# Optimization experiments

Measured on AMD Instinct MI355X. Metric: run time of the kernel, lower is better.

Reference implementation:

```python
import jax, jax.numpy as jnp
import numpy as np

B, D, L, E, H = 8192, 1024, 256, 16, 400

def setup_inputs() -> dict:
    key = jax.random.key(0)
    ks = jax.random.split(key, 6)
    s1 = 1.0 / np.sqrt(D)
    s2 = 1.0 / np.sqrt(H)
    return {
        "x": jax.random.normal(ks[0], (B, D), dtype=jnp.float32),
        "angle_idx": jax.random.randint(ks[1], (B,), 0, E, dtype=jnp.int64),
        "W1": jax.random.uniform(ks[2], (E, D, H), jnp.float32, -s1, s1),
        "b1": jax.random.uniform(ks[3], (E, H), jnp.float32, -s1, s1),
        "W2": jax.random.uniform(ks[4], (E, H, 2 * L), jnp.float32, -s2, s2),
        "b2": jax.random.uniform(ks[5], (E, 2 * L), jnp.float32, -s2, s2),
    }

def reference(x, angle_idx, W1, b1, W2, b2):
    # Dense all-experts compute, then per-sample select (jit-friendly MoE dispatch).
    # h1: [E, B, H]
    h1 = jax.nn.relu(jnp.einsum('bd,edh->ebh', x, W1) + b1[:, None, :])
    # h: [E, B, 2L]
    h = jnp.einsum('ebh,ehk->ebk', h1, W2) + b2[:, None, :]
    sel = h[angle_idx, jnp.arange(x.shape[0])]  # [B, 2L], each row from its routed expert
    half = sel.shape[1] // 2
    z_mu, z_logvar = sel[:, :half], sel[:, half:]
    return (z_mu, z_logvar)
```

## Files before the change

### kernel.cpp

```cpp
#include <hip/hip_runtime.h>
#include <hip/hip_bf16.h>
#include <cstdint>
#include <cstddef>

#define B_N 8192
#define D_K 1024
#define H_N 400
#define HP  416
#define K2_N 512
#define E_N 16
#define L_N 256
#define TM 64
#define PAD_ROWS (B_N + E_N * TM)
#define NTILES (PAD_ROWS / TM)

typedef short bf16x8 __attribute__((ext_vector_type(8)));
typedef float f32x4 __attribute__((ext_vector_type(4)));

#define GLDS(gp, lp) __builtin_amdgcn_global_load_lds( \
    (const __attribute__((address_space(1))) unsigned int*)(gp), \
    (__attribute__((address_space(3))) unsigned int*)(lp), 16, 0, 0)

static __device__ __forceinline__ unsigned short f2bf(float f) {
  union { float f; unsigned int u; } c; c.f = f;
  unsigned int u = c.u + 0x7fffu + ((c.u >> 16) & 1u);
  return (unsigned short)(u >> 16);
}
static __device__ __forceinline__ unsigned int pkbf(float a, float b) {
  union { __hip_bfloat162 v; unsigned int u; } c;
  c.v = __float22bfloat162_rn(make_float2(a, b));
  return c.u;
}

__global__ __launch_bounds__(256) void hist_kernel(const int* __restrict__ idx,
                                                   int* __restrict__ hist) {
  __shared__ int h[E_N];
  const int t = threadIdx.x;
  if (t < E_N) h[t] = 0;
  __syncthreads();
  atomicAdd(&h[idx[blockIdx.x * 256 + t]], 1);
  __syncthreads();
  if (t < E_N) hist[blockIdx.x * E_N + t] = h[t];
}

__global__ __launch_bounds__(256) void prep_kernel(const float* __restrict__ W1,
                                                   const float* __restrict__ W2,
                                                   const float* __restrict__ x,
                                                   const int* __restrict__ idx,
                                                   const int* __restrict__ hist,
                                                   unsigned short* __restrict__ Wt1,
                                                   unsigned short* __restrict__ Wt2,
                                                   unsigned short* __restrict__ xc,
                                                   int* __restrict__ off_al,
                                                   int* __restrict__ cnt_al,
                                                   int* __restrict__ order) {
  const int bid = blockIdx.x;
  const int t = threadIdx.x;
  if (bid < 2688) {
    __shared__ unsigned short Ls[64][72];
    const float* S; unsigned short* Dt; int K, N, Kd, Nd, k0, n0;
    if (bid < 1792) {
      int e = bid / 112, r = bid % 112;
      k0 = (r % 16) * 64; n0 = (r / 16) * 64;
      S = W1 + (size_t)e * D_K * H_N; Dt = Wt1 + (size_t)e * HP * D_K;
      K = D_K; N = H_N; Kd = D_K; Nd = HP;
    } else {
      int t2 = bid - 1792; int e = t2 / 56, r = t2 % 56;
      k0 = (r % 7) * 64; n0 = (r / 7) * 64;
      S = W2 + (size_t)e * H_N * K2_N; Dt = Wt2 + (size_t)e * K2_N * HP;
      K = H_N; N = K2_N; Kd = HP; Nd = K2_N;
    }
    const int kk = t >> 4;
    const int nn = (t & 15) * 4;
    float4 v[4];
#pragma unroll
    for (int p = 0; p < 4; ++p) {
      int k = k0 + p * 16 + kk;
      int n = n0 + nn;
      v[p] = make_float4(0.f, 0.f, 0.f, 0.f);
      if (k < K && n + 3 < N) v[p] = *(const float4*)(S + (size_t)k * N + n);
    }
#pragma unroll
    for (int p = 0; p < 4; ++p) {
      Ls[nn + 0][p * 16 + kk] = f2bf(v[p].x);
      Ls[nn + 1][p * 16 + kk] = f2bf(v[p].y);
      Ls[nn + 2][p * 16 + kk] = f2bf(v[p].z);
      Ls[nn + 3][p * 16 + kk] = f2bf(v[p].w);
    }
    __syncthreads();
    const int n2 = t >> 3;
    const int ch = t & 7;
#pragma unroll
    for (int p = 0; p < 2; ++p) {
      int n = n0 + p * 32 + n2;
      int k = k0 + ch * 8;
      if (n < Nd && k < Kd)
        *(uint4*)(Dt + (size_t)n * Kd + k) = *(const uint4*)&Ls[p * 32 + n2][ch * 8];
    }
  } else if (bid < 3200) {
    const int xb = bid - 2688;
    const float* S = x + (size_t)xb * 16 * D_K;
    unsigned short* Dp = xc + (size_t)xb * 16 * D_K;
#pragma unroll
    for (int i = 0; i < 16; ++i) {
      float4 v = *(const float4*)(S + i * D_K + t * 4);
      uint2 o; o.x = pkbf(v.x, v.y); o.y = pkbf(v.z, v.w);
      *(uint2*)(Dp + i * D_K + t * 4) = o;
    }
  } else {
    const int hb = bid - 3200;
    __shared__ int totL[E_N], preL[E_N], offsL[E_N], curL[E_N];
    if (t < E_N) {
      int pre = 0, tot = 0;
      for (int b = 0; b < 32; ++b) {
        int h = hist[b * E_N + t];
        if (b < hb) pre += h;
        tot += h;
      }
      totL[t] = tot; preL[t] = pre;
    }
    __syncthreads();
    if (t == 0) {
      int acc = 0;
      for (int e = 0; e < E_N; ++e) {
        offsL[e] = acc;
        if (hb == 0) off_al[e] = acc;
        acc += ((totL[e] + TM - 1) / TM) * TM;
      }
      if (hb == 0) off_al[E_N] = acc;
    }
    __syncthreads();
    if (t < E_N) {
      curL[t] = offsL[t] + preL[t];
      if (hb == 0) cnt_al[t] = totL[t];
    }
    __syncthreads();
    const int b = hb * 256 + t;
    const int e = idx[b];
    const int slot = atomicAdd(&curL[e], 1);
    order[slot] = b;
    if (hb == 0) *(uint2*)(xc + (size_t)B_N * D_K + t * 4) = make_uint2(0, 0);
  }
}

__global__ __launch_bounds__(256) void gemm1_kernel(const unsigned short* __restrict__ xc,
                                                    const unsigned short* __restrict__ Wt1,
                                                    const float* __restrict__ b1,
                                                    const int* __restrict__ off_al,
                                                    const int* __restrict__ cnt_al,
                                                    const int* __restrict__ order,
                                                    unsigned short* __restrict__ h1buf) {
  __shared__ unsigned short As[2][64 * 32];
  __shared__ unsigned short Bs[2][128 * 32];
  __shared__ int offs[E_N + 1];
  __shared__ int rowidx[TM];
  const int tid = threadIdx.x;
  const int m0 = blockIdx.x * TM;
  const int nb = blockIdx.y;
  if (tid <= E_N) offs[tid] = off_al[tid];
  __syncthreads();
  if (m0 >= offs[E_N]) return;
  int e = 0;
  while (m0 >= offs[e + 1]) ++e;
  if (tid < TM) {
    const bool valid = (m0 + tid) < (offs[e] + cnt_al[e]);
    rowidx[tid] = valid ? order[m0 + tid] : B_N;
  }
  __syncthreads();
  const unsigned short* Wt1e = Wt1 + (size_t)e * HP * D_K;

  const int l = tid & 63, w = tid >> 6;
  const int r4 = l >> 2;
  const int sg = (r4 ^ (r4 >> 2)) & 3;
  const int g8 = ((l & 3) ^ sg) * 8;
  const int t0 = nb * 8 + 2 * w;
  const bool act0 = (t0 < 25);
  const bool act1 = (t0 + 1 < 25);
  const unsigned short* gA = xc + (size_t)rowidx[16 * w + r4] * D_K + g8;
  const unsigned short* gB0 = Wt1e + (size_t)(t0 * 16 + r4) * D_K + g8;
  const unsigned short* gB1 = gB0 + (size_t)16 * D_K;

  const int ln = l & 15, q = l >> 4;
  const int sr = (ln ^ (ln >> 2)) & 3;
  const int cq = (q ^ sr) * 8;

  f32x4 acc[4][2] = {};

  GLDS(gA, &As[0][16 * w * 32]);
  if (act0) GLDS(gB0, &Bs[0][(2 * w + 0) * 512]);
  if (act1) GLDS(gB1, &Bs[0][(2 * w + 1) * 512]);

  for (int k0 = 0; k0 < D_K; k0 += 32) {
    const int cur = (k0 >> 5) & 1;
    const int nxt = cur ^ 1;
    __syncthreads();
    if (k0 + 32 < D_K) {
      GLDS(gA + k0 + 32, &As[nxt][16 * w * 32]);
      if (act0) GLDS(gB0 + k0 + 32, &Bs[nxt][(2 * w + 0) * 512]);
      if (act1) GLDS(gB1 + k0 + 32, &Bs[nxt][(2 * w + 1) * 512]);
    }
    if (act0) {
      bf16x8 af[4];
#pragma unroll
      for (int i = 0; i < 4; ++i)
        af[i] = *(const bf16x8*)&As[cur][(16 * i + ln) * 32 + cq];
      bf16x8 b0f = *(const bf16x8*)&Bs[cur][(2 * w + 0) * 512 + ln * 32 + cq];
#pragma unroll
      for (int i = 0; i < 4; ++i)
        acc[i][0] = __builtin_amdgcn_mfma_f32_16x16x32_bf16(b0f, af[i], acc[i][0], 0, 0, 0);
      if (act1) {
        bf16x8 b1f = *(const bf16x8*)&Bs[cur][(2 * w + 1) * 512 + ln * 32 + cq];
#pragma unroll
        for (int i = 0; i < 4; ++i)
          acc[i][1] = __builtin_amdgcn_mfma_f32_16x16x32_bf16(b1f, af[i], acc[i][1], 0, 0, 0);
      }
    }
  }

#pragma unroll
  for (int j = 0; j < 2; ++j) {
    if (j == 0 ? act0 : act1) {
      const int n4 = (t0 + j) * 16 + 4 * q;
      const float4 bv = *(const float4*)&b1[e * H_N + n4];
#pragma unroll
      for (int i = 0; i < 4; ++i) {
        const size_t m = (size_t)(m0 + 16 * i + ln);
        uint2 o;
        o.x = pkbf(fmaxf(acc[i][j][0] + bv.x, 0.f), fmaxf(acc[i][j][1] + bv.y, 0.f));
        o.y = pkbf(fmaxf(acc[i][j][2] + bv.z, 0.f), fmaxf(acc[i][j][3] + bv.w, 0.f));
        *(uint2*)&h1buf[m * HP + n4] = o;
      }
    }
  }
}

__global__ __launch_bounds__(256) void gemm2_kernel(const unsigned short* __restrict__ h1buf,
                                                    const unsigned short* __restrict__ Wt2,
                                                    const float* __restrict__ b2,
                                                    const int* __restrict__ off_al,
                                                    const int* __restrict__ cnt_al,
                                                    const int* __restrict__ order,
                                                    float* __restrict__ out) {
  __shared__ unsigned short As[2][64 * 32];
  __shared__ unsigned short Bs[2][128 * 32];
  __shared__ int offs[E_N + 1];
  __shared__ int rowidx[TM];
  const int tid = threadIdx.x;
  const int m0 = blockIdx.x * TM;
  const int nb = blockIdx.y;
  if (tid <= E_N) offs[tid] = off_al[tid];
  __syncthreads();
  if (m0 >= offs[E_N]) return;
  int e = 0;
  while (m0 >= offs[e + 1]) ++e;
  if (tid < TM) {
    const bool valid = (m0 + tid) < (offs[e] + cnt_al[e]);
    rowidx[tid] = valid ? order[m0 + tid] : -1;
  }
  __syncthreads();
  const unsigned short* Wt2e = Wt2 + (size_t)e * K2_N * HP;

  const int l = tid & 63, w = tid >> 6;
  const int r4 = l >> 2;
  const int sg = (r4 ^ (r4 >> 2)) & 3;
  const int g8 = ((l & 3) ^ sg) * 8;
  const int t0 = nb * 8 + 2 * w;
  const unsigned short* gA = h1buf + (size_t)(m0 + 16 * w + r4) * HP + g8;
  const unsigned short* gB0 = Wt2e + (size_t)(t0 * 16 + r4) * HP + g8;
  const unsigned short* gB1 = gB0 + (size_t)16 * HP;

  const int ln = l & 15, q = l >> 4;
  const int sr = (ln ^ (ln >> 2)) & 3;
  const int cq = (q ^ sr) * 8;

  f32x4 acc[4][2] = {};

  GLDS(gA, &As[0][16 * w * 32]);
  GLDS(gB0, &Bs[0][(2 * w + 0) * 512]);
  GLDS(gB1, &Bs[0][(2 * w + 1) * 512]);

  for (int k0 = 0; k0 < HP; k0 += 32) {
    const int cur = (k0 >> 5) & 1;
    const int nxt = cur ^ 1;
    __syncthreads();
    if (k0 + 32 < HP) {
      GLDS(gA + k0 + 32, &As[nxt][16 * w * 32]);
      GLDS(gB0 + k0 + 32, &Bs[nxt][(2 * w + 0) * 512]);
      GLDS(gB1 + k0 + 32, &Bs[nxt][(2 * w + 1) * 512]);
    }
    bf16x8 af[4];
#pragma unroll
    for (int i = 0; i < 4; ++i)
      af[i] = *(const bf16x8*)&As[cur][(16 * i + ln) * 32 + cq];
    bf16x8 b0f = *(const bf16x8*)&Bs[cur][(2 * w + 0) * 512 + ln * 32 + cq];
#pragma unroll
    for (int i = 0; i < 4; ++i)
      acc[i][0] = __builtin_amdgcn_mfma_f32_16x16x32_bf16(b0f, af[i], acc[i][0], 0, 0, 0);
    bf16x8 b1f = *(const bf16x8*)&Bs[cur][(2 * w + 1) * 512 + ln * 32 + cq];
#pragma unroll
    for (int i = 0; i < 4; ++i)
      acc[i][1] = __builtin_amdgcn_mfma_f32_16x16x32_bf16(b1f, af[i], acc[i][1], 0, 0, 0);
  }

#pragma unroll
  for (int j = 0; j < 2; ++j) {
    const int n4 = (t0 + j) * 16 + 4 * q;
    const float4 bv = *(const float4*)&b2[e * K2_N + n4];
#pragma unroll
    for (int i = 0; i < 4; ++i) {
      const int s = rowidx[16 * i + ln];
      if (s >= 0) {
        float4 v;
        v.x = acc[i][j][0] + bv.x;
        v.y = acc[i][j][1] + bv.y;
        v.z = acc[i][j][2] + bv.z;
        v.w = acc[i][j][3] + bv.w;
        if (n4 < L_N) *(float4*)&out[(size_t)s * L_N + n4] = v;
        else          *(float4*)&out[(size_t)(B_N + s) * L_N + (n4 - L_N)] = v;
      }
    }
  }
}

extern "C" void kernel_launch(void* const* d_in, const int* in_sizes, int n_in,
                              void* d_out, int out_size, void* d_ws, size_t ws_size,
                              hipStream_t stream) {
  const float* x   = (const float*)d_in[0];
  const int*   idx = (const int*)d_in[1];
  const float* W1  = (const float*)d_in[2];
  const float* b1  = (const float*)d_in[3];
  const float* W2  = (const float*)d_in[4];
  const float* b2  = (const float*)d_in[5];
  float* out = (float*)d_out;

  char* ws = (char*)d_ws;
  int* off_al = (int*)(ws + 0);
  int* cnt_al = (int*)(ws + 128);
  int* hist   = (int*)(ws + 192);
  int* order  = (int*)(ws + 2240);
  unsigned short* xc  = (unsigned short*)(ws + 39104);
  unsigned short* h1  = (unsigned short*)(ws + 16818368);
  unsigned short* Wt1 = (unsigned short*)(ws + 24486080);
  unsigned short* Wt2 = (unsigned short*)(ws + 38117568);

  hist_kernel<<<32, 256, 0, stream>>>(idx, hist);
  prep_kernel<<<3232, 256, 0, stream>>>(W1, W2, x, idx, hist, Wt1, Wt2, xc,
                                        off_al, cnt_al, order);
  gemm1_kernel<<<dim3(NTILES, 4), 256, 0, stream>>>(xc, Wt1, b1, off_al, cnt_al, order, h1);
  gemm2_kernel<<<dim3(NTILES, 4), 256, 0, stream>>>(h1, Wt2, b2, off_al, cnt_al, order, out);
}
```

Baseline: 163.5 us.

## Fuse both expert GEMMs into one kernel keeping h1 in LDS

Merges gemm1 and gemm2 into a single mlp_kernel. Each 32-row tile computes the full 400-wide hidden activation into shared memory, then runs the second GEMM from LDS. This removes the global h1 round trip and one launch. The histogram kernel is also folded into prep, with each scan block recounting idx itself, and the tile grid is remapped with a block-index swizzle. In exchange each block reloads the whole expert weights for only 32 rows, with fewer blocks and more LDS per block, which may lower weight reuse and occupancy.

```diff
diff --git a/kernel.cpp b/kernel.cpp
--- a/kernel.cpp
+++ b/kernel.cpp
@@ -7,12 +7,13 @@
 #define D_K 1024
 #define H_N 400
 #define HP  416
+#define HPAD 424
 #define K2_N 512
 #define E_N 16
 #define L_N 256
-#define TM 64
-#define PAD_ROWS (B_N + E_N * TM)
-#define NTILES (PAD_ROWS / TM)
+#define TMR 32
+#define PAD_ROWS (B_N + E_N * TMR)
+#define NT2 (PAD_ROWS / TMR)
 
 typedef short bf16x8 __attribute__((ext_vector_type(8)));
 typedef float f32x4 __attribute__((ext_vector_type(4)));
@@ -32,22 +33,10 @@
   return c.u;
 }
 
-__global__ __launch_bounds__(256) void hist_kernel(const int* __restrict__ idx,
-                                                   int* __restrict__ hist) {
-  __shared__ int h[E_N];
-  const int t = threadIdx.x;
-  if (t < E_N) h[t] = 0;
-  __syncthreads();
-  atomicAdd(&h[idx[blockIdx.x * 256 + t]], 1);
-  __syncthreads();
-  if (t < E_N) hist[blockIdx.x * E_N + t] = h[t];
-}
-
 __global__ __launch_bounds__(256) void prep_kernel(const float* __restrict__ W1,
                                                    const float* __restrict__ W2,
                                                    const float* __restrict__ x,
                                                    const int* __restrict__ idx,
-                                                   const int* __restrict__ hist,
                                                    unsigned short* __restrict__ Wt1,
                                                    unsigned short* __restrict__ Wt2,
                                                    unsigned short* __restrict__ xc,
@@ -110,14 +99,13 @@
   } else {
     const int hb = bid - 3200;
     __shared__ int totL[E_N], preL[E_N], offsL[E_N], curL[E_N];
-    if (t < E_N) {
-      int pre = 0, tot = 0;
-      for (int b = 0; b < 32; ++b) {
-        int h = hist[b * E_N + t];
-        if (b < hb) pre += h;
-        tot += h;
-      }
-      totL[t] = tot; preL[t] = pre;
+    if (t < E_N) { totL[t] = 0; preL[t] = 0; }
+    __syncthreads();
+    const int lim = hb * 256;
+    for (int i = t; i < B_N; i += 256) {
+      const int e0 = idx[i];
+      atomicAdd(&totL[e0], 1);
+      if (i < lim) atomicAdd(&preL[e0], 1);
     }
     __syncthreads();
     if (t == 0) {
@@ -125,7 +113,7 @@
       for (int e = 0; e < E_N; ++e) {
         offsL[e] = acc;
         if (hb == 0) off_al[e] = acc;
-        acc += ((totL[e] + TM - 1) / TM) * TM;
+        acc += ((totL[e] + TMR - 1) / TMR) * TMR;
       }
       if (hb == 0) off_al[E_N] = acc;
     }
@@ -143,182 +131,151 @@
   }
 }
 
-__global__ __launch_bounds__(256) void gemm1_kernel(const unsigned short* __restrict__ xc,
-                                                    const unsigned short* __restrict__ Wt1,
-                                                    const float* __restrict__ b1,
-                                                    const int* __restrict__ off_al,
-                                                    const int* __restrict__ cnt_al,
-                                                    const int* __restrict__ order,
-                                                    unsigned short* __restrict__ h1buf) {
-  __shared__ unsigned short As[2][64 * 32];
-  __shared__ unsigned short Bs[2][128 * 32];
+__global__ __launch_bounds__(256) void mlp_kernel(
+    const unsigned short* __restrict__ xc,
+    const unsigned short* __restrict__ Wt1,
+    const unsigned short* __restrict__ Wt2,
+    const float* __restrict__ b1, const float* __restrict__ b2,
+    const int* __restrict__ off_al, const int* __restrict__ cnt_al,
+    const int* __restrict__ order, float* __restrict__ out) {
+  __shared__ unsigned short h1s[TMR * HPAD];
+  __shared__ unsigned short Bs[2 * 13 * 512];
+  __shared__ unsigned short As[2 * 2 * 512];
   __shared__ int offs[E_N + 1];
-  __shared__ int rowidx[TM];
-  const int tid = threadIdx.x;
-  const int m0 = blockIdx.x * TM;
-  const int nb = blockIdx.y;
-  if (tid <= E_N) offs[tid] = off_al[tid];
+  __shared__ int rowidx[TMR];
+  const int t = threadIdx.x;
+  const int vid = (blockIdx.x & 7) * 34 + (blockIdx.x >> 3);
+  const int m0 = vid * TMR;
+  if (t <= E_N) offs[t] = off_al[t];
   __syncthreads();
   if (m0 >= offs[E_N]) return;
   int e = 0;
   while (m0 >= offs[e + 1]) ++e;
-  if (tid < TM) {
-    const bool valid = (m0 + tid) < (offs[e] + cnt_al[e]);
-    rowidx[tid] = valid ? order[m0 + tid] : B_N;
+  if (t < TMR) {
+    const bool valid = (m0 + t) < (offs[e] + cnt_al[e]);
+    rowidx[t] = valid ? order[m0 + t] : -1;
+  }
+  for (int z = t; z < TMR * 12; z += 256) {
+    const int row = z / 12, c2 = z % 12;
+    *(unsigned int*)&h1s[row * HPAD + 400 + c2 * 2] = 0u;
   }
   __syncthreads();
+
+  const int l = t & 63, w = t >> 6;
+  const int r4 = l >> 2;
+  const int sgx = (r4 ^ (r4 >> 2)) & 3;
+  const int g8 = ((l & 3) ^ sgx) * 8;
+  const int ln = l & 15, q = l >> 4;
+  const int srx = (ln ^ (ln >> 2)) & 3;
+  const int cq = (q ^ srx) * 8;
+
+  const int ar = (w < 2) ? rowidx[16 * w + r4] : -1;
+  const unsigned short* gA = xc + (size_t)(ar < 0 ? B_N : ar) * D_K + g8;
   const unsigned short* Wt1e = Wt1 + (size_t)e * HP * D_K;
-
-  const int l = tid & 63, w = tid >> 6;
-  const int r4 = l >> 2;
-  const int sg = (r4 ^ (r4 >> 2)) & 3;
-  const int g8 = ((l & 3) ^ sg) * 8;
-  const int t0 = nb * 8 + 2 * w;
-  const bool act0 = (t0 < 25);
-  const bool act1 = (t0 + 1 < 25);
-  const unsigned short* gA = xc + (size_t)rowidx[16 * w + r4] * D_K + g8;
-  const unsigned short* gB0 = Wt1e + (size_t)(t0 * 16 + r4) * D_K + g8;
-  const unsigned short* gB1 = gB0 + (size_t)16 * D_K;
-
-  const int ln = l & 15, q = l >> 4;
-  const int sr = (ln ^ (ln >> 2)) & 3;
-  const int cq = (q ^ sr) * 8;
-
-  f32x4 acc[4][2] = {};
-
-  GLDS(gA, &As[0][16 * w * 32]);
-  if (act0) GLDS(gB0, &Bs[0][(2 * w + 0) * 512]);
-  if (act1) GLDS(gB1, &Bs[0][(2 * w + 1) * 512]);
-
-  for (int k0 = 0; k0 < D_K; k0 += 32) {
-    const int cur = (k0 >> 5) & 1;
-    const int nxt = cur ^ 1;
-    __syncthreads();
-    if (k0 + 32 < D_K) {
-      GLDS(gA + k0 + 32, &As[nxt][16 * w * 32]);
-      if (act0) GLDS(gB0 + k0 + 32, &Bs[nxt][(2 * w + 0) * 512]);
-      if (act1) GLDS(gB1 + k0 + 32, &Bs[nxt][(2 * w + 1) * 512]);
-    }
-    if (act0) {
-      bf16x8 af[4];
-#pragma unroll
-      for (int i = 0; i < 4; ++i)
-        af[i] = *(const bf16x8*)&As[cur][(16 * i + ln) * 32 + cq];
-      bf16x8 b0f = *(const bf16x8*)&Bs[cur][(2 * w + 0) * 512 + ln * 32 + cq];
-#pragma unroll
-      for (int i = 0; i < 4; ++i)
-        acc[i][0] = __builtin_amdgcn_mfma_f32_16x16x32_bf16(b0f, af[i], acc[i][0], 0, 0, 0);
-      if (act1) {
-        bf16x8 b1f = *(const bf16x8*)&Bs[cur][(2 * w + 1) * 512 + ln * 32 + cq];
-#pragma unroll
-        for (int i = 0; i < 4; ++i)
-          acc[i][1] = __builtin_amdgcn_mfma_f32_16x16x32_bf16(b1f, af[i], acc[i][1], 0, 0, 0);
-      }
-    }
-  }
-
-#pragma unroll
-  for (int j = 0; j < 2; ++j) {
-    if (j == 0 ? act0 : act1) {
-      const int n4 = (t0 + j) * 16 + 4 * q;
-      const float4 bv = *(const float4*)&b1[e * H_N + n4];
-#pragma unroll
-      for (int i = 0; i < 4; ++i) {
-        const size_t m = (size_t)(m0 + 16 * i + ln);
-        uint2 o;
-        o.x = pkbf(fmaxf(acc[i][j][0] + bv.x, 0.f), fmaxf(acc[i][j][1] + bv.y, 0.f));
-        o.y = pkbf(fmaxf(acc[i][j][2] + bv.z, 0.f), fmaxf(acc[i][j][3] + bv.w, 0.f));
-        *(uint2*)&h1buf[m * HP + n4] = o;
-      }
-    }
-  }
-}
-
-__global__ __launch_bounds__(256) void gemm2_kernel(const unsigned short* __restrict__ h1buf,
-                                                    const unsigned short* __restrict__ Wt2,
-                                                    const float* __restrict__ b2,
-                                                    const int* __restrict__ off_al,
-                                                    const int* __restrict__ cnt_al,
-                                                    const int* __restrict__ order,
-                                                    float* __restrict__ out) {
-  __shared__ unsigned short As[2][64 * 32];
-  __shared__ unsigned short Bs[2][128 * 32];
-  __shared__ int offs[E_N + 1];
-  __shared__ int rowidx[TM];
-  const int tid = threadIdx.x;
-  const int m0 = blockIdx.x * TM;
-  const int nb = blockIdx.y;
-  if (tid <= E_N) offs[tid] = off_al[tid];
+  const unsigned short* Wt2e = Wt2 + (size_t)e * K2_N * HP;
+
+#pragma unroll 1
+  for (int pass = 0; pass < 2; ++pass) {
+    const int tstart = pass ? 13 : 0;
+    const int tcnt = pass ? 12 : 13;
+    const int nj = (tcnt - w + 3) >> 2;
+    const unsigned short* gB[4];
+#pragma unroll
+    for (int j = 0; j < 4; ++j)
+      gB[j] = Wt1e + (size_t)((tstart + w + 4 * j) * 16 + r4) * D_K + g8;
+    f32x4 acc[4][2] = {};
+    if (w < 2) GLDS(gA, &As[w * 512]);
+#pragma unroll
+    for (int j = 0; j < 4; ++j)
+      if (j < nj) GLDS(gB[j], &Bs[(w + 4 * j) * 512]);
+    for (int k0 = 0; k0 < D_K; k0 += 32) {
+      const int cur = (k0 >> 5) & 1, nxt = cur ^ 1;
+      __syncthreads();
+      if (k0 + 32 < D_K) {
+        if (w < 2) GLDS(gA + k0 + 32, &As[(nxt * 2 + w) * 512]);
+#pragma unroll
+        for (int j = 0; j < 4; ++j)
+          if (j < nj) GLDS(gB[j] + k0 + 32, &Bs[(nxt * 13 + w + 4 * j) * 512]);
+      }
+      const bf16x8 af0 = *(const bf16x8*)&As[(cur * 2 + 0) * 512 + ln * 32 + cq];
+      const bf16x8 af1 = *(const bf16x8*)&As[(cur * 2 + 1) * 512 + ln * 32 + cq];
+#pragma unroll
+      for (int j = 0; j < 4; ++j)
+        if (j < nj) {
+          const bf16x8 bf = *(const bf16x8*)&Bs[(cur * 13 + w + 4 * j) * 512 + ln * 32 + cq];
+          acc[j][0] = __builtin_amdgcn_mfma_f32_16x16x32_bf16(bf, af0, acc[j][0], 0, 0, 0);
+          acc[j][1] = __builtin_amdgcn_mfma_f32_16x16x32_bf16(bf, af1, acc[j][1], 0, 0, 0);
+        }
+    }
+    __syncthreads();
+#pragma unroll
+    for (int j = 0; j < 4; ++j)
+      if (j < nj) {
+        const int n4 = (tstart + w + 4 * j) * 16 + 4 * q;
+        const float4 bv = *(const float4*)&b1[e * H_N + n4];
+#pragma unroll
+        for (int i = 0; i < 2; ++i) {
+          const int m = 16 * i + ln;
+          uint2 o;
+          o.x = pkbf(fmaxf(acc[j][i][0] + bv.x, 0.f), fmaxf(acc[j][i][1] + bv.y, 0.f));
+          o.y = pkbf(fmaxf(acc[j][i][2] + bv.z, 0.f), fmaxf(acc[j][i][3] + bv.w, 0.f));
+          *(uint2*)&h1s[m * HPAD + n4] = o;
+        }
+      }
+  }
   __syncthreads();
-  if (m0 >= offs[E_N]) return;
-  int e = 0;
-  while (m0 >= offs[e + 1]) ++e;
-  if (tid < TM) {
-    const bool valid = (m0 + tid) < (offs[e] + cnt_al[e]);
-    rowidx[tid] = valid ? order[m0 + tid] : -1;
-  }
-  __syncthreads();
-  const unsigned short* Wt2e = Wt2 + (size_t)e * K2_N * HP;
-
-  const int l = tid & 63, w = tid >> 6;
-  const int r4 = l >> 2;
-  const int sg = (r4 ^ (r4 >> 2)) & 3;
-  const int g8 = ((l & 3) ^ sg) * 8;
-  const int t0 = nb * 8 + 2 * w;
-  const unsigned short* gA = h1buf + (size_t)(m0 + 16 * w + r4) * HP + g8;
-  const unsigned short* gB0 = Wt2e + (size_t)(t0 * 16 + r4) * HP + g8;
-  const unsigned short* gB1 = gB0 + (size_t)16 * HP;
-
-  const int ln = l & 15, q = l >> 4;
-  const int sr = (ln ^ (ln >> 2)) & 3;
-  const int cq = (q ^ sr) * 8;
-
-  f32x4 acc[4][2] = {};
-
-  GLDS(gA, &As[0][16 * w * 32]);
-  GLDS(gB0, &Bs[0][(2 * w + 0) * 512]);
-  GLDS(gB1, &Bs[0][(2 * w + 1) * 512]);
-
-  for (int k0 = 0; k0 < HP; k0 += 32) {
-    const int cur = (k0 >> 5) & 1;
-    const int nxt = cur ^ 1;
-    __syncthreads();
-    if (k0 + 32 < HP) {
-      GLDS(gA + k0 + 32, &As[nxt][16 * w * 32]);
-      GLDS(gB0 + k0 + 32, &Bs[nxt][(2 * w + 0) * 512]);
-      GLDS(gB1 + k0 + 32, &Bs[nxt][(2 * w + 1) * 512]);
-    }
-    bf16x8 af[4];
-#pragma unroll
-    for (int i = 0; i < 4; ++i)
-      af[i] = *(const bf16x8*)&As[cur][(16 * i + ln) * 32 + cq];
-    bf16x8 b0f = *(const bf16x8*)&Bs[cur][(2 * w + 0) * 512 + ln * 32 + cq];
-#pragma unroll
-    for (int i = 0; i < 4; ++i)
-      acc[i][0] = __builtin_amdgcn_mfma_f32_16x16x32_bf16(b0f, af[i], acc[i][0], 0, 0, 0);
-    bf16x8 b1f = *(const bf16x8*)&Bs[cur][(2 * w + 1) * 512 + ln * 32 + cq];
-#pragma unroll
-    for (int i = 0; i < 4; ++i)
-      acc[i][1] = __builtin_amdgcn_mfma_f32_16x16x32_bf16(b1f, af[i], acc[i][1], 0, 0, 0);
-  }
-
-#pragma unroll
-  for (int j = 0; j < 2; ++j) {
-    const int n4 = (t0 + j) * 16 + 4 * q;
-    const float4 bv = *(const float4*)&b2[e * K2_N + n4];
-#pragma unroll
-    for (int i = 0; i < 4; ++i) {
-      const int s = rowidx[16 * i + ln];
-      if (s >= 0) {
-        float4 v;
-        v.x = acc[i][j][0] + bv.x;
-        v.y = acc[i][j][1] + bv.y;
-        v.z = acc[i][j][2] + bv.z;
-        v.w = acc[i][j][3] + bv.w;
-        if (n4 < L_N) *(float4*)&out[(size_t)s * L_N + n4] = v;
-        else          *(float4*)&out[(size_t)(B_N + s) * L_N + (n4 - L_N)] = v;
-      }
-    }
+
+#pragma unroll 1
+  for (int pass = 0; pass < 3; ++pass) {
+    const int tstart = pass * 13;
+    const int tcnt = (pass == 2) ? 6 : 13;
+    const int nj = (tcnt > w) ? ((tcnt - w + 3) >> 2) : 0;
+    const unsigned short* gB[4];
+#pragma unroll
+    for (int j = 0; j < 4; ++j)
+      gB[j] = Wt2e + (size_t)((tstart + w + 4 * j) * 16 + r4) * HP + g8;
+    f32x4 acc[4][2] = {};
+#pragma unroll
+    for (int j = 0; j < 4; ++j)
+      if (j < nj) GLDS(gB[j], &Bs[(w + 4 * j) * 512]);
+    for (int k0 = 0; k0 < HP; k0 += 32) {
+      const int cur = (k0 >> 5) & 1, nxt = cur ^ 1;
+      __syncthreads();
+      if (k0 + 32 < HP) {
+#pragma unroll
+        for (int j = 0; j < 4; ++j)
+          if (j < nj) GLDS(gB[j] + k0 + 32, &Bs[(nxt * 13 + w + 4 * j) * 512]);
+      }
+      const bf16x8 af0 = *(const bf16x8*)&h1s[(0 + ln) * HPAD + k0 + q * 8];
+      const bf16x8 af1 = *(const bf16x8*)&h1s[(16 + ln) * HPAD + k0 + q * 8];
+#pragma unroll
+      for (int j = 0; j < 4; ++j)
+        if (j < nj) {
+          const bf16x8 bf = *(const bf16x8*)&Bs[(cur * 13 + w + 4 * j) * 512 + ln * 32 + cq];
+          acc[j][0] = __builtin_amdgcn_mfma_f32_16x16x32_bf16(bf, af0, acc[j][0], 0, 0, 0);
+          acc[j][1] = __builtin_amdgcn_mfma_f32_16x16x32_bf16(bf, af1, acc[j][1], 0, 0, 0);
+        }
+    }
+    __syncthreads();
+#pragma unroll
+    for (int j = 0; j < 4; ++j)
+      if (j < nj) {
+        const int n4 = (tstart + w + 4 * j) * 16 + 4 * q;
+        const float4 bv = *(const float4*)&b2[e * K2_N + n4];
+#pragma unroll
+        for (int i = 0; i < 2; ++i) {
+          const int s = rowidx[16 * i + ln];
+          if (s >= 0) {
+            float4 v;
+            v.x = acc[j][i][0] + bv.x;
+            v.y = acc[j][i][1] + bv.y;
+            v.z = acc[j][i][2] + bv.z;
+            v.w = acc[j][i][3] + bv.w;
+            if (n4 < L_N) *(float4*)&out[(size_t)s * L_N + n4] = v;
+            else          *(float4*)&out[(size_t)(B_N + s) * L_N + (n4 - L_N)] = v;
+          }
+        }
+      }
   }
 }
 
@@ -336,16 +293,13 @@
   char* ws = (char*)d_ws;
   int* off_al = (int*)(ws + 0);
   int* cnt_al = (int*)(ws + 128);
-  int* hist   = (int*)(ws + 192);
   int* order  = (int*)(ws + 2240);
   unsigned short* xc  = (unsigned short*)(ws + 39104);
-  unsigned short* h1  = (unsigned short*)(ws + 16818368);
   unsigned short* Wt1 = (unsigned short*)(ws + 24486080);
   unsigned short* Wt2 = (unsigned short*)(ws + 38117568);
 
-  hist_kernel<<<32, 256, 0, stream>>>(idx, hist);
-  prep_kernel<<<3232, 256, 0, stream>>>(W1, W2, x, idx, hist, Wt1, Wt2, xc,
+  prep_kernel<<<3232, 256, 0, stream>>>(W1, W2, x, idx, Wt1, Wt2, xc,
                                         off_al, cnt_al, order);
-  gemm1_kernel<<<dim3(NTILES, 4), 256, 0, stream>>>(xc, Wt1, b1, off_al, cnt_al, order, h1);
-  gemm2_kernel<<<dim3(NTILES, 4), 256, 0, stream>>>(h1, Wt2, b2, off_al, cnt_al, order, out);
-}
+  mlp_kernel<<<NT2, 256, 0, stream>>>(xc, Wt1, Wt2, b1, b2,
+                                      off_al, cnt_al, order, out);
+}
```

Result: slower. 183.0 us (+11.9%).
